# Optimization experiments

Measured on AMD Instinct MI355X. Metric: run time of the kernel, lower is better.

The kernel has to match this reference:

```python
import jax, jax.numpy as jnp
import numpy as np

N, F, F_, H = 8192, 128, 64, 4
NEG = -1e10  # K.constant(-10000000000.0) mask value


def setup_inputs() -> dict:
    key = jax.random.key(0)
    k1, k2, k3, k4, k5 = jax.random.split(key, 5)
    X = jax.random.normal(k1, (N, F), dtype=jnp.float32)
    A = jax.random.randint(k2, (N, N), 0, 2).astype(jnp.float32)
    W = jax.random.normal(k3, (H, F, F_), dtype=jnp.float32) * 0.1
    a_self = jax.random.normal(k4, (H, F_), dtype=jnp.float32) * 0.1
    a_neigh = jax.random.normal(k5, (H, F_), dtype=jnp.float32) * 0.1
    return {"X": X, "A": A, "W": W, "a_self": a_self, "a_neigh": a_neigh}


def reference(X, A, W, a_self, a_neigh):
    # per-head linear projection: [H, N, F_]
    Xp = jnp.einsum('nf,hfd->hnd', X, W)
    # additive attention scores
    s_self = jnp.einsum('hnd,hd->hn', Xp, a_self)    # [H, N]
    s_neigh = jnp.einsum('hnd,hd->hn', Xp, a_neigh)  # [H, N]
    dense = s_self[:, :, None] + s_neigh[:, None, :]  # [H, N, N]
    dense = jnp.where(dense > 0, dense, 0.2 * dense)  # LeakyReLU(0.2)
    mask = jnp.where(A == 0.0, jnp.float32(NEG), jnp.float32(0.0))  # [N, N]
    attn = jax.nn.softmax(dense + mask[None], axis=-1)  # [H, N, N]
    # dropout on attention coeffs is identity at inference
    feats = jnp.einsum('hnm,hmd->hnd', attn, Xp)  # [H, N, F_]
    feats = jax.nn.relu(feats)  # activation applied per head before concat
    # concat heads -> [N, H*F_]
    return jnp.transpose(feats, (1, 0, 2)).reshape(N, H * F_)
```

## Files before the change

kernel.cpp:

```cpp
#include <hip/hip_runtime.h>
#include <stdint.h>


#define NN    8192
#define FF    128
#define FD    64
#define HH    4
#define SPLIT 8
#define KT_PER_SPLIT ((NN / SPLIT) / 32)
#define LOG2E 1.4426950408889634f

typedef __attribute__((ext_vector_type(8))) short short8;
typedef __attribute__((ext_vector_type(4))) float f32x4;

extern "C" __device__ float __ocml_exp2_f32(float);

__device__ __forceinline__ float fast_exp2(float x) {
#if __has_builtin(__builtin_amdgcn_exp2f)
    return __builtin_amdgcn_exp2f(x);
#else
    return __ocml_exp2_f32(x);
#endif
}

__device__ __forceinline__ float bf16_to_f32(unsigned short u) {
    return __builtin_bit_cast(float, ((unsigned)u) << 16);
}
__device__ __forceinline__ unsigned f32_to_bf16_rne(float f) {
    unsigned u = __builtin_bit_cast(unsigned, f);
    u = (u + 0x7FFFu + ((u >> 16) & 1u)) >> 16;
    return u;
}
__device__ __forceinline__ unsigned pack_bf16_trunc(float lo, float hi) {
    return __builtin_amdgcn_perm(__builtin_bit_cast(unsigned, hi),
                                 __builtin_bit_cast(unsigned, lo), 0x07060302u);
}
__device__ __forceinline__ void async_load16(const void* g, void* l) {
    __builtin_amdgcn_global_load_lds(
        (const __attribute__((address_space(1))) unsigned int*)g,
        (__attribute__((address_space(3))) unsigned int*)l, 16, 0, 0);
}

#define WS_XPT   0
#define WS_U     (WS_XPT + HH * FD * NN * 2)
#define WS_V     (WS_U + HH * NN * 4)
#define WS_VC    (WS_V + HH * NN * 4)
#define WS_M     (WS_VC + HH * NN * 4)
#define WS_WT    (WS_M + 256)
#define WS_ACCP  (WS_WT + HH * FD * FF * 2)
#define WS_LP    (WS_ACCP + (size_t)SPLIT * HH * NN * FD * 2)

__global__ void k0_transpose_w(const float* __restrict__ W,
                               unsigned short* __restrict__ WT) {
    int b = blockIdx.x;
    int h = b >> 3, fb = b & 7;
    int t = threadIdx.x;
    int d = t & 63, fo = t >> 6;
    #pragma unroll
    for (int i = 0; i < 4; ++i) {
        int f = fb * 16 + fo * 4 + i;
        WT[(h * FD + d) * FF + f] = (unsigned short)f32_to_bf16_rne(W[(h * FF + f) * FD + d]);
    }
}

__global__ __launch_bounds__(256) void k1_project(
        const float* __restrict__ X,
        const unsigned short* __restrict__ WT,
        const float* __restrict__ a_self,
        const float* __restrict__ a_neigh,
        unsigned short* __restrict__ XpT,
        float* __restrict__ U, float* __restrict__ V) {
    __shared__ __align__(16) char XsB[64 * 272];
    __shared__ __align__(16) char WsB[64 * 272];
    const int rb = blockIdx.x * 64;
    const int h  = blockIdx.y;
    const int t  = threadIdx.x;
    const float4* xs = (const float4*)(X + (size_t)rb * FF);
    #pragma unroll
    for (int i = 0; i < 8; ++i) {
        int c = i * 256 + t;
        float4 v = xs[c];
        uint2 pv;
        pv.x = f32_to_bf16_rne(v.x) | (f32_to_bf16_rne(v.y) << 16);
        pv.y = f32_to_bf16_rne(v.z) | (f32_to_bf16_rne(v.w) << 16);
        *(uint2*)(XsB + (c >> 5) * 272 + (c & 31) * 8) = pv;
    }
    const uint4* wsrc = (const uint4*)(WT + (size_t)h * FD * FF);
    #pragma unroll
    for (int i = 0; i < 4; ++i) {
        int c = i * 256 + t;
        *(uint4*)(WsB + (c >> 4) * 272 + (c & 15) * 16) = wsrc[c];
    }
    __syncthreads();
    const int lane = t & 63, wid = t >> 6;
    const int r15 = lane & 15, quad = lane >> 4;
    const int lrow = wid * 16 + r15;

    f32x4 acc[4];
    #pragma unroll
    for (int cg = 0; cg < 4; ++cg) acc[cg] = (f32x4){0.f, 0.f, 0.f, 0.f};
    #pragma unroll
    for (int kt = 0; kt < 4; ++kt) {
        short8 afr = *(const short8*)(XsB + lrow * 272 + kt * 64 + quad * 16);
        #pragma unroll
        for (int cg = 0; cg < 4; ++cg) {
            short8 bfr = *(const short8*)(WsB + (cg * 16 + r15) * 272 + kt * 64 + quad * 16);
            acc[cg] = __builtin_amdgcn_mfma_f32_16x16x32_bf16(afr, bfr, acc[cg], 0, 0, 0);
        }
    }
    float as[4], an[4];
    #pragma unroll
    for (int cg = 0; cg < 4; ++cg) {
        as[cg] = a_self[h * FD + cg * 16 + r15];
        an[cg] = a_neigh[h * FD + cg * 16 + r15];
    }
    #pragma unroll
    for (int reg = 0; reg < 4; ++reg) {
        float s1 = 0.f, s2 = 0.f;
        #pragma unroll
        for (int cg = 0; cg < 4; ++cg) { s1 += acc[cg][reg] * as[cg]; s2 += acc[cg][reg] * an[cg]; }
        #pragma unroll
        for (int m = 1; m <= 8; m <<= 1) { s1 += __shfl_xor(s1, m); s2 += __shfl_xor(s2, m); }
        if (r15 == 0) {
            int n = rb + wid * 16 + quad * 4 + reg;
            U[h * NN + n] = s1;
            V[h * NN + n] = s2;
        }
    }
    #pragma unroll
    for (int cg = 0; cg < 4; ++cg) {
        uint2 val;
        val.x = f32_to_bf16_rne(acc[cg][0]) | (f32_to_bf16_rne(acc[cg][1]) << 16);
        val.y = f32_to_bf16_rne(acc[cg][2]) | (f32_to_bf16_rne(acc[cg][3]) << 16);
        int d = cg * 16 + r15;
        int n0 = rb + wid * 16 + quad * 4;
        *(uint2*)((char*)XpT + ((size_t)(h * FD + d) * NN + n0) * 2) = val;
    }
}

__global__ void k1b_max(const float* __restrict__ U, const float* __restrict__ V,
                        float* __restrict__ Vc, float* __restrict__ M) {
    int h = blockIdx.x, t = threadIdx.x;
    __shared__ float red[256];
    float mu = -1e30f, mv = -1e30f;
    for (int i = t; i < NN; i += 256) {
        mu = fmaxf(mu, U[h * NN + i]);
        mv = fmaxf(mv, V[h * NN + i]);
    }
    red[t] = mu; __syncthreads();
    for (int s = 128; s > 0; s >>= 1) { if (t < s) red[t] = fmaxf(red[t], red[t + s]); __syncthreads(); }
    float Mu = red[0]; __syncthreads();
    red[t] = mv; __syncthreads();
    for (int s = 128; s > 0; s >>= 1) { if (t < s) red[t] = fmaxf(red[t], red[t + s]); __syncthreads(); }
    float Mv = red[0];
    if (t == 0) M[h] = Mu + Mv;
    for (int i = t; i < NN; i += 256) Vc[h * NN + i] = V[h * NN + i] * LOG2E;
}

__global__ __launch_bounds__(256, 3) void k2_attend(
        const float* __restrict__ Ag,
        const unsigned short* __restrict__ XpT,
        const float* __restrict__ U, const float* __restrict__ Vc,
        const float* __restrict__ Mbuf,
        unsigned short* __restrict__ accP,
        float* __restrict__ lP) {
    __shared__ __align__(16) char Xsb[2][16384];
    const int t = threadIdx.x;
    const int lane = t & 63, wid = t >> 6;
    const int r15 = lane & 15, quad = lane >> 4;
    const int rb = blockIdx.x * 64;
    const int sp = blockIdx.y;
    const int h = wid;

    const float mh = Mbuf[h];
    const float qoff = -0.8f * mh * LOG2E;
    float u1g[4];
    #pragma unroll
    for (int g = 0; g < 4; ++g)
        u1g[g] = (U[h * NN + rb + g * 16 + r15] - mh) * LOG2E;

    f32x4 acc[4][4];
    #pragma unroll
    for (int g = 0; g < 4; ++g)
        #pragma unroll
        for (int cg = 0; cg < 4; ++cg) acc[g][cg] = (f32x4){0.f, 0.f, 0.f, 0.f};
    float lsum[4] = {0.f, 0.f, 0.f, 0.f};

    const int kb0 = sp * (NN / SPLIT);
    const int srow = wid * 64 + (lane >> 2);
    const int sc   = (lane & 3) ^ ((lane >> 3) & 3);
    const char* sbase = (const char*)XpT + ((size_t)srow * NN + kb0 + sc * 8) * 2;
    const size_t irow_step = (size_t)16 * NN * 2;
    #pragma unroll
    for (int i = 0; i < 4; ++i)
        async_load16(sbase + (size_t)i * irow_step, &Xsb[0][(wid * 4 + i) * 1024]);

    const float* aB = Ag + (size_t)rb * NN + kb0;
    const int swz = (quad ^ ((r15 >> 1) & 3)) * 16;

    #pragma unroll 2
    for (int kt = 0; kt < KT_PER_SPLIT; ++kt) {
        const int cur = kt & 1;
        __syncthreads();
        if (kt + 1 < KT_PER_SPLIT) {
            const char* sb2 = sbase + (size_t)(kt + 1) * 64;
            #pragma unroll
            for (int i = 0; i < 4; ++i)
                async_load16(sb2 + (size_t)i * irow_step, &Xsb[cur ^ 1][(wid * 4 + i) * 1024]);
        }
        const int kb = kt * 32;
        float4 a0[4], a1[4];
        #pragma unroll
        for (int g = 0; g < 4; ++g) {
            const float* ar = aB + (size_t)(g * 16 + r15) * NN + kb + quad * 8;
            a0[g] = *(const float4*)(ar);
            a1[g] = *(const float4*)(ar + 4);
        }
        const float* vr = Vc + h * NN + kb0 + kb + quad * 8;
        float4 va  = *(const float4*)(vr);
        float4 vb2 = *(const float4*)(vr + 4);
        short8 bfr[4];
        #pragma unroll
        for (int cg = 0; cg < 4; ++cg)
            bfr[cg] = *(const short8*)(&Xsb[cur][(h * FD + cg * 16 + r15) * 64 + swz]);

        #pragma unroll
        for (int g = 0; g < 4; ++g) {
            float w[8];
            #pragma unroll
            for (int j = 0; j < 4; ++j) {
                float p = u1g[g] + ((const float*)&va)[j];
                float q = fmaf(0.2f, p, qoff);
                w[j] = fast_exp2(fmaxf(p, q)) * ((const float*)&a0[g])[j];
            }
            #pragma unroll
            for (int j = 0; j < 4; ++j) {
                float p = u1g[g] + ((const float*)&vb2)[j];
                float q = fmaf(0.2f, p, qoff);
                w[4 + j] = fast_exp2(fmaxf(p, q)) * ((const float*)&a1[g])[j];
            }
            lsum[g] += ((w[0] + w[1]) + (w[2] + w[3])) + ((w[4] + w[5]) + (w[6] + w[7]));
            uint4 pkv;
            pkv.x = pack_bf16_trunc(w[0], w[1]);
            pkv.y = pack_bf16_trunc(w[2], w[3]);
            pkv.z = pack_bf16_trunc(w[4], w[5]);
            pkv.w = pack_bf16_trunc(w[6], w[7]);
            short8 afrag = __builtin_bit_cast(short8, pkv);
            #pragma unroll
            for (int cg = 0; cg < 4; ++cg)
                acc[g][cg] = __builtin_amdgcn_mfma_f32_16x16x32_bf16(afrag, bfr[cg], acc[g][cg], 0, 0, 0);
        }
    }
    #pragma unroll
    for (int g = 0; g < 4; ++g) {
        lsum[g] += __shfl_xor(lsum[g], 16);
        lsum[g] += __shfl_xor(lsum[g], 32);
    }
    if (lane < 16) {
        #pragma unroll
        for (int g = 0; g < 4; ++g)
            lP[(size_t)(sp * HH + h) * NN + rb + g * 16 + lane] = lsum[g];
    }
    #pragma unroll
    for (int g = 0; g < 4; ++g)
        #pragma unroll
        for (int cg = 0; cg < 4; ++cg) {
            int d = cg * 16 + r15;
            #pragma unroll
            for (int reg = 0; reg < 4; ++reg) {
                int n = rb + g * 16 + quad * 4 + reg;
                accP[((size_t)(sp * HH + h) * NN + n) * FD + d] =
                    (unsigned short)f32_to_bf16_rne(acc[g][cg][reg]);
            }
        }
}

__global__ void k3_combine(const unsigned short* __restrict__ accP,
                           const float* __restrict__ lP,
                           float* __restrict__ out) {
    int e = blockIdx.x * 256 + threadIdx.x;
    int n = e >> 8, c = e & 255;
    int h = c >> 6, d = c & 63;
    float num = 0.f, den = 0.f;
    #pragma unroll
    for (int s = 0; s < SPLIT; ++s) {
        num += bf16_to_f32(accP[((size_t)(s * HH + h) * NN + n) * FD + d]);
        den += lP[(size_t)(s * HH + h) * NN + n];
    }
    out[e] = fmaxf(num * __builtin_amdgcn_rcpf(den), 0.f);
}

extern "C" void kernel_launch(void* const* d_in, const int* in_sizes, int n_in,
                              void* d_out, int out_size, void* d_ws, size_t ws_size,
                              hipStream_t stream) {
    (void)in_sizes; (void)n_in; (void)out_size; (void)ws_size;
    const float* X       = (const float*)d_in[0];
    const float* A       = (const float*)d_in[1];
    const float* W       = (const float*)d_in[2];
    const float* a_self  = (const float*)d_in[3];
    const float* a_neigh = (const float*)d_in[4];
    char* ws = (char*)d_ws;
    unsigned short* XpT  = (unsigned short*)(ws + WS_XPT);
    float*          U    = (float*)(ws + WS_U);
    float*          V    = (float*)(ws + WS_V);
    float*          Vc   = (float*)(ws + WS_VC);
    float*          M    = (float*)(ws + WS_M);
    unsigned short* WT   = (unsigned short*)(ws + WS_WT);
    unsigned short* accP = (unsigned short*)(ws + WS_ACCP);
    float*          lP   = (float*)(ws + WS_LP);
    float*          out  = (float*)d_out;

    k0_transpose_w<<<dim3(32), dim3(256), 0, stream>>>(W, WT);
    k1_project<<<dim3(NN / 64, HH), dim3(256), 0, stream>>>(X, WT, a_self, a_neigh, XpT, U, V);
    k1b_max<<<dim3(HH), dim3(256), 0, stream>>>(U, V, Vc, M);
    k2_attend<<<dim3(NN / 64, SPLIT), dim3(256), 0, stream>>>(A, XpT, U, Vc, M, accP, lP);
    k3_combine<<<dim3(NN), dim3(256), 0, stream>>>(accP, lP, out);
}
```

Measured before the change: 538.3 us.

## Fuse max reduction into projection via atomics; stage adjacency tiles through LDS asynchronously

Drops the separate k1b_max kernel. Projection blocks now compute per-wave maxima of the self and neighbour scores and merge them with atomicMax on order-preserving unsigned keys, and the log2e scaling of V moves into the attention loop. In the attention kernel, adjacency tiles are loaded asynchronously into a swizzled, double-buffered LDS buffer, and V is prefetched one step ahead instead of read directly from global memory each iteration. This removes one launch and the serialized reduction pass, and overlaps adjacency fetch with compute, at the cost of extra LDS per block, which may affect occupancy.

```diff
diff --git a/kernel.cpp b/kernel.cpp
--- a/kernel.cpp
+++ b/kernel.cpp
@@ -40,21 +40,30 @@
         (const __attribute__((address_space(1))) unsigned int*)g,
         (__attribute__((address_space(3))) unsigned int*)l, 16, 0, 0);
 }
+__device__ __forceinline__ unsigned enc_key(float f) {
+    unsigned u = __builtin_bit_cast(unsigned, f);
+    return (u & 0x80000000u) ? ~u : (u | 0x80000000u);
+}
+__device__ __forceinline__ float dec_key(unsigned k) {
+    unsigned u = (k & 0x80000000u) ? (k ^ 0x80000000u) : ~k;
+    return __builtin_bit_cast(float, u);
+}
 
 #define WS_XPT   0
 #define WS_U     (WS_XPT + HH * FD * NN * 2)
 #define WS_V     (WS_U + HH * NN * 4)
-#define WS_VC    (WS_V + HH * NN * 4)
-#define WS_M     (WS_VC + HH * NN * 4)
-#define WS_WT    (WS_M + 256)
+#define WS_MK    (WS_V + HH * NN * 4)
+#define WS_WT    (WS_MK + 256)
 #define WS_ACCP  (WS_WT + HH * FD * FF * 2)
 #define WS_LP    (WS_ACCP + (size_t)SPLIT * HH * NN * FD * 2)
 
 __global__ void k0_transpose_w(const float* __restrict__ W,
-                               unsigned short* __restrict__ WT) {
+                               unsigned short* __restrict__ WT,
+                               unsigned* __restrict__ MK) {
     int b = blockIdx.x;
+    int t = threadIdx.x;
+    if (b == 0 && t < 8) MK[t] = 0u;
     int h = b >> 3, fb = b & 7;
-    int t = threadIdx.x;
     int d = t & 63, fo = t >> 6;
     #pragma unroll
     for (int i = 0; i < 4; ++i) {
@@ -69,7 +78,8 @@
         const float* __restrict__ a_self,
         const float* __restrict__ a_neigh,
         unsigned short* __restrict__ XpT,
-        float* __restrict__ U, float* __restrict__ V) {
+        float* __restrict__ U, float* __restrict__ V,
+        unsigned* __restrict__ MK) {
     __shared__ __align__(16) char XsB[64 * 272];
     __shared__ __align__(16) char WsB[64 * 272];
     const int rb = blockIdx.x * 64;
@@ -114,6 +124,7 @@
         as[cg] = a_self[h * FD + cg * 16 + r15];
         an[cg] = a_neigh[h * FD + cg * 16 + r15];
     }
+    float mu = -1e30f, mv = -1e30f;
     #pragma unroll
     for (int reg = 0; reg < 4; ++reg) {
         float s1 = 0.f, s2 = 0.f;
@@ -121,11 +132,18 @@
         for (int cg = 0; cg < 4; ++cg) { s1 += acc[cg][reg] * as[cg]; s2 += acc[cg][reg] * an[cg]; }
         #pragma unroll
         for (int m = 1; m <= 8; m <<= 1) { s1 += __shfl_xor(s1, m); s2 += __shfl_xor(s2, m); }
+        mu = fmaxf(mu, s1); mv = fmaxf(mv, s2);
         if (r15 == 0) {
             int n = rb + wid * 16 + quad * 4 + reg;
             U[h * NN + n] = s1;
             V[h * NN + n] = s2;
         }
+    }
+    mu = fmaxf(mu, __shfl_xor(mu, 16)); mu = fmaxf(mu, __shfl_xor(mu, 32));
+    mv = fmaxf(mv, __shfl_xor(mv, 16)); mv = fmaxf(mv, __shfl_xor(mv, 32));
+    if (lane == 0) {
+        atomicMax(&MK[h], enc_key(mu));
+        atomicMax(&MK[4 + h], enc_key(mv));
     }
     #pragma unroll
     for (int cg = 0; cg < 4; ++cg) {
@@ -138,46 +156,29 @@
     }
 }
 
-__global__ void k1b_max(const float* __restrict__ U, const float* __restrict__ V,
-                        float* __restrict__ Vc, float* __restrict__ M) {
-    int h = blockIdx.x, t = threadIdx.x;
-    __shared__ float red[256];
-    float mu = -1e30f, mv = -1e30f;
-    for (int i = t; i < NN; i += 256) {
-        mu = fmaxf(mu, U[h * NN + i]);
-        mv = fmaxf(mv, V[h * NN + i]);
-    }
-    red[t] = mu; __syncthreads();
-    for (int s = 128; s > 0; s >>= 1) { if (t < s) red[t] = fmaxf(red[t], red[t + s]); __syncthreads(); }
-    float Mu = red[0]; __syncthreads();
-    red[t] = mv; __syncthreads();
-    for (int s = 128; s > 0; s >>= 1) { if (t < s) red[t] = fmaxf(red[t], red[t + s]); __syncthreads(); }
-    float Mv = red[0];
-    if (t == 0) M[h] = Mu + Mv;
-    for (int i = t; i < NN; i += 256) Vc[h * NN + i] = V[h * NN + i] * LOG2E;
-}
-
 __global__ __launch_bounds__(256, 3) void k2_attend(
         const float* __restrict__ Ag,
         const unsigned short* __restrict__ XpT,
-        const float* __restrict__ U, const float* __restrict__ Vc,
-        const float* __restrict__ Mbuf,
+        const float* __restrict__ U, const float* __restrict__ V,
+        const unsigned* __restrict__ MK,
         unsigned short* __restrict__ accP,
         float* __restrict__ lP) {
     __shared__ __align__(16) char Xsb[2][16384];
+    __shared__ __align__(16) char Asb[2][8192];
     const int t = threadIdx.x;
     const int lane = t & 63, wid = t >> 6;
     const int r15 = lane & 15, quad = lane >> 4;
     const int rb = blockIdx.x * 64;
     const int sp = blockIdx.y;
     const int h = wid;
-
-    const float mh = Mbuf[h];
-    const float qoff = -0.8f * mh * LOG2E;
+    const int kb0 = sp * (NN / SPLIT);
+
+    const float M = dec_key(MK[h]) + dec_key(MK[4 + h]);
+    const float qoff = -0.8f * M * LOG2E;
     float u1g[4];
     #pragma unroll
     for (int g = 0; g < 4; ++g)
-        u1g[g] = (U[h * NN + rb + g * 16 + r15] - mh) * LOG2E;
+        u1g[g] = (U[h * NN + rb + g * 16 + r15] - M) * LOG2E;
 
     f32x4 acc[4][4];
     #pragma unroll
@@ -186,58 +187,71 @@
         for (int cg = 0; cg < 4; ++cg) acc[g][cg] = (f32x4){0.f, 0.f, 0.f, 0.f};
     float lsum[4] = {0.f, 0.f, 0.f, 0.f};
 
-    const int kb0 = sp * (NN / SPLIT);
-    const int srow = wid * 64 + (lane >> 2);
-    const int sc   = (lane & 3) ^ ((lane >> 3) & 3);
-    const char* sbase = (const char*)XpT + ((size_t)srow * NN + kb0 + sc * 8) * 2;
-    const size_t irow_step = (size_t)16 * NN * 2;
+    const int srX = wid * 64 + (lane >> 2);
+    const int scX = (lane & 3) ^ ((lane >> 3) & 3);
+    const char* xsrc = (const char*)XpT + ((size_t)srX * NN + kb0 + scX * 8) * 2;
+    const size_t xstep = (size_t)16 * NN * 2;
+    const int rA = wid * 16 + (lane >> 3);
+    const int chA = (lane & 7) ^ (((rA >> 1) & 3) << 1);
+    const float* asrc = Ag + (size_t)(rb + rA) * NN + kb0 + chA * 4;
+    const size_t astep = (size_t)8 * NN;
+
     #pragma unroll
     for (int i = 0; i < 4; ++i)
-        async_load16(sbase + (size_t)i * irow_step, &Xsb[0][(wid * 4 + i) * 1024]);
-
-    const float* aB = Ag + (size_t)rb * NN + kb0;
-    const int swz = (quad ^ ((r15 >> 1) & 3)) * 16;
+        async_load16(xsrc + (size_t)i * xstep, &Xsb[0][(wid * 4 + i) * 1024]);
+    #pragma unroll
+    for (int i = 0; i < 2; ++i)
+        async_load16(asrc + i * astep, &Asb[0][(wid * 2 + i) * 1024]);
+
+    const float* vbase = V + h * NN + kb0 + quad * 8;
+    float4 vg[2][2];
+    vg[0][0] = *(const float4*)(vbase);
+    vg[0][1] = *(const float4*)(vbase + 4);
+
+    const int swzX = (quad ^ ((r15 >> 1) & 3)) * 16;
+    const int swzA = (quad ^ ((r15 >> 1) & 3)) * 32;
 
     #pragma unroll 2
     for (int kt = 0; kt < KT_PER_SPLIT; ++kt) {
-        const int cur = kt & 1;
+        const int cur = kt & 1, nxt = cur ^ 1;
         __syncthreads();
         if (kt + 1 < KT_PER_SPLIT) {
-            const char* sb2 = sbase + (size_t)(kt + 1) * 64;
+            const char*  xs2 = xsrc + (size_t)(kt + 1) * 64;
+            const float* as2 = asrc + (size_t)(kt + 1) * 32;
             #pragma unroll
             for (int i = 0; i < 4; ++i)
-                async_load16(sb2 + (size_t)i * irow_step, &Xsb[cur ^ 1][(wid * 4 + i) * 1024]);
-        }
-        const int kb = kt * 32;
-        float4 a0[4], a1[4];
+                async_load16(xs2 + (size_t)i * xstep, &Xsb[nxt][(wid * 4 + i) * 1024]);
+            #pragma unroll
+            for (int i = 0; i < 2; ++i)
+                async_load16(as2 + i * astep, &Asb[nxt][(wid * 2 + i) * 1024]);
+        }
+        {
+            const int ktn = (kt + 1 < KT_PER_SPLIT) ? kt + 1 : kt;
+            vg[nxt][0] = *(const float4*)(vbase + ktn * 32);
+            vg[nxt][1] = *(const float4*)(vbase + ktn * 32 + 4);
+        }
+        short8 bfr[4];
+        #pragma unroll
+        for (int cg = 0; cg < 4; ++cg)
+            bfr[cg] = *(const short8*)(&Xsb[cur][(h * FD + cg * 16 + r15) * 64 + swzX]);
+
         #pragma unroll
         for (int g = 0; g < 4; ++g) {
-            const float* ar = aB + (size_t)(g * 16 + r15) * NN + kb + quad * 8;
-            a0[g] = *(const float4*)(ar);
-            a1[g] = *(const float4*)(ar + 4);
-        }
-        const float* vr = Vc + h * NN + kb0 + kb + quad * 8;
-        float4 va  = *(const float4*)(vr);
-        float4 vb2 = *(const float4*)(vr + 4);
-        short8 bfr[4];
-        #pragma unroll
-        for (int cg = 0; cg < 4; ++cg)
-            bfr[cg] = *(const short8*)(&Xsb[cur][(h * FD + cg * 16 + r15) * 64 + swz]);
-
-        #pragma unroll
-        for (int g = 0; g < 4; ++g) {
+            const char* arow = &Asb[cur][(g * 16 + r15) * 128 + swzA];
+            f32x4 a0 = *(const f32x4*)(arow);
+            f32x4 a1 = *(const f32x4*)(arow + 16);
             float w[8];
             #pragma unroll
             for (int j = 0; j < 4; ++j) {
-                float p = u1g[g] + ((const float*)&va)[j];
+                float p = fmaf(((const float*)&vg[cur][0])[j], LOG2E, u1g[g]);
                 float q = fmaf(0.2f, p, qoff);
-                w[j] = fast_exp2(fmaxf(p, q)) * ((const float*)&a0[g])[j];
+                w[j] = fast_exp2(fmaxf(p, q)) * a0[j];
             }
             #pragma unroll
             for (int j = 0; j < 4; ++j) {
-                float p = u1g[g] + ((const float*)&vb2)[j];
+                float p = fmaf(((const float*)&vg[cur][1])[j], LOG2E, u1g[g]);
                 float q = fmaf(0.2f, p, qoff);
-                w[4 + j] = fast_exp2(fmaxf(p, q)) * ((const float*)&a1[g])[j];
+                w[4 + j] = fast_exp2(fmaxf(p, q)) * a1[j];
             }
             lsum[g] += ((w[0] + w[1]) + (w[2] + w[3])) + ((w[4] + w[5]) + (w[6] + w[7]));
             uint4 pkv;
@@ -303,16 +317,14 @@
     unsigned short* XpT  = (unsigned short*)(ws + WS_XPT);
     float*          U    = (float*)(ws + WS_U);
     float*          V    = (float*)(ws + WS_V);
-    float*          Vc   = (float*)(ws + WS_VC);
-    float*          M    = (float*)(ws + WS_M);
+    unsigned*       MK   = (unsigned*)(ws + WS_MK);
     unsigned short* WT   = (unsigned short*)(ws + WS_WT);
     unsigned short* accP = (unsigned short*)(ws + WS_ACCP);
     float*          lP   = (float*)(ws + WS_LP);
     float*          out  = (float*)d_out;
 
-    k0_transpose_w<<<dim3(32), dim3(256), 0, stream>>>(W, WT);
-    k1_project<<<dim3(NN / 64, HH), dim3(256), 0, stream>>>(X, WT, a_self, a_neigh, XpT, U, V);
-    k1b_max<<<dim3(HH), dim3(256), 0, stream>>>(U, V, Vc, M);
-    k2_attend<<<dim3(NN / 64, SPLIT), dim3(256), 0, stream>>>(A, XpT, U, Vc, M, accP, lP);
+    k0_transpose_w<<<dim3(32), dim3(256), 0, stream>>>(W, WT, MK);
+    k1_project<<<dim3(NN / 64, HH), dim3(256), 0, stream>>>(X, WT, a_self, a_neigh, XpT, U, V, MK);
+    k2_attend<<<dim3(NN / 64, SPLIT), dim3(256), 0, stream>>>(A, XpT, U, V, MK, accP, lP);
     k3_combine<<<dim3(NN), dim3(256), 0, stream>>>(accP, lP, out);
 }
```

Result: faster. 506.2 us (-6.0%).
